# Kernel tuning notes

Hardware: AMD Instinct MI355X
Metric: run time of the kernel (lower is better)

Reference implementation:

```python
import jax, jax.numpy as jnp
import numpy as np

N = 4096          # leng_doc (number of tokens)
D_S = 70          # DEP_EMB_DIM + 2*BI_LSTM_PHASE_1_OUTPUT_DIM = 10 + 60

def setup_inputs() -> dict:
    key = jax.random.key(0)
    k1, k2 = jax.random.split(key)
    adj = jax.random.uniform(k1, (N, N, 2), dtype=jnp.float32)   # unweighted adjacency, 2 edge directions/channels
    s = jax.random.normal(k2, (N, D_S), dtype=jnp.float32)       # per-node edge-representation s
    return {"adj": adj, "s": s}

def reference(adj, s):
    # Faithful to CalculateHLayer-style math (CalculateSLayer analog):
    #   s_in[j,d]  = sum_i sum_k adj[i,j,k] * s[i,d]
    #   s_out[i,d] = sum_j sum_k adj[i,j,k] * s[j,d]
    # Sum over the channel axis k first, then contract the node axis with a GEMM
    # instead of materializing the (N,N,2,D) broadcast intermediate.
    a = adj.sum(axis=2)                 # (N, N)
    s_in = jnp.einsum('ij,id->jd', a, s)   # reduce over source nodes -> (N, D)
    s_out = jnp.einsum('ij,jd->id', a, s)  # reduce over target nodes -> (N, D)
    return (s_in, s_out)
```

## Files before the change

kernel.cpp:

```cpp
#include <hip/hip_runtime.h>


#define N    4096
#define D    70
#define DP   80
#define TILE 128
#define NT_D 5
#define NPART 32
#define ATP  132
#define SJP  136

typedef short short8  __attribute__((ext_vector_type(8)));
typedef short short4v __attribute__((ext_vector_type(4)));
typedef float f32x4   __attribute__((ext_vector_type(4)));

__device__ __forceinline__ unsigned short f2bf(float f) {
    unsigned u = __builtin_bit_cast(unsigned, f);
    u += 0x7FFFu + ((u >> 16) & 1u);
    return (unsigned short)(u >> 16);
}
__device__ __forceinline__ float bf2f(unsigned short h) {
    unsigned u = (unsigned)h << 16;
    return __builtin_bit_cast(float, u);
}
__device__ __forceinline__ short8 ld_b64x2(const unsigned short* p) {
    short4v lo = *(const short4v*)p;
    short4v hi = *(const short4v*)(p + 4);
    return __builtin_shufflevector(lo, hi, 0, 1, 2, 3, 4, 5, 6, 7);
}

__global__ __launch_bounds__(256) void build_sT(const float* __restrict__ s,
                                                unsigned short* __restrict__ sT) {
    __shared__ unsigned short tile[DP][264];
    const int t  = threadIdx.x;
    const int n0 = blockIdx.x * 256;
    #pragma unroll
    for (int d = 0; d < D; ++d)
        tile[d][t] = f2bf(s[(size_t)(n0 + t) * D + d]);
    __syncthreads();
    #pragma unroll
    for (int d = 0; d < DP; ++d) {
        unsigned short v = (d < D) ? tile[d][t] : (unsigned short)0;
        sT[(size_t)d * N + n0 + t] = v;
    }
}

template<bool USE_WS>
__global__ __launch_bounds__(512, 4) void fused_slayer(
    const float* __restrict__ adj,
    const unsigned short* __restrict__ sT,
    unsigned short* __restrict__ wsi,
    unsigned short* __restrict__ wso,
    float* __restrict__ out)
{
    __shared__ __align__(16) unsigned short a_row[2][TILE][40];
    __shared__ __align__(16) unsigned short aTt[2][32][ATP];
    __shared__ __align__(16) unsigned short sTj[DP][SJP];

    const int t    = threadIdx.x;
    const int lane = t & 63;
    const int w    = t >> 6;
    const int l16  = lane & 15;
    const int q    = lane >> 4;
    const int bx   = blockIdx.x;
    const int by   = blockIdx.y;
    const int I0   = by * TILE;
    const int J0   = bx * TILE;

    #pragma unroll
    for (int p = 0; p < 3; ++p) {
        int ii = t + 512 * p;
        if (ii < DP * 16) {
            int d = ii >> 4, c = ii & 15;
            *(uint4*)&sTj[d][8 * c] = *(const uint4*)(sT + (size_t)d * N + J0 + 8 * c);
        }
    }

    const int slot_mt = w & 1;
    const int slot_nt = w >> 1;
    const bool extra  = (w < 2);
    short8 bfi[4], bfe[4];
    {
        const int d = 16 * slot_nt + l16;
        #pragma unroll
        for (int ks = 0; ks < 4; ++ks)
            bfi[ks] = *(const short8*)(sT + (size_t)d * N + I0 + 32 * ks + 8 * q);
        if (extra) {
            const int d2 = 64 + l16;
            #pragma unroll
            for (int ks = 0; ks < 4; ++ks)
                bfe[ks] = *(const short8*)(sT + (size_t)d2 * N + I0 + 32 * ks + 8 * q);
        }
    }

    const f32x4 zero = {0.0f, 0.0f, 0.0f, 0.0f};
    f32x4 acc1[NT_D];
    #pragma unroll
    for (int nt = 0; nt < NT_D; ++nt) acc1[nt] = zero;

    const int jp = t & 15;
    const int ir = t >> 4;

    float4 v[4];
    #pragma unroll
    for (int it = 0; it < 4; ++it) {
        int i = 32 * it + ir;
        v[it] = *(const float4*)(adj + (size_t)(I0 + i) * (2 * N)
                                     + (size_t)(J0 + 2 * jp) * 2);
    }

    #pragma unroll
    for (int jc = 0; jc < 4; ++jc) {
        const int b = jc & 1;

        #pragma unroll
        for (int it = 0; it < 4; ++it) {
            int i = 32 * it + ir;
            unsigned short b0 = f2bf(v[it].x + v[it].y);
            unsigned short b1 = f2bf(v[it].z + v[it].w);
            *(unsigned int*)&a_row[b][i][2 * jp] =
                (unsigned int)b0 | ((unsigned int)b1 << 16);
            aTt[b][2 * jp][i]     = b0;
            aTt[b][2 * jp + 1][i] = b1;
        }
        __syncthreads();

        if (jc < 3) {
            #pragma unroll
            for (int it = 0; it < 4; ++it) {
                int i = 32 * it + ir;
                v[it] = *(const float4*)(adj + (size_t)(I0 + i) * (2 * N)
                                             + (size_t)(J0 + 32 * (jc + 1) + 2 * jp) * 2);
            }
        }

        {
            short8 af = *(const short8*)&a_row[b][16 * w + l16][8 * q];
            #pragma unroll
            for (int nt = 0; nt < NT_D; ++nt) {
                short8 bf = *(const short8*)&sTj[16 * nt + l16][32 * jc + 8 * q];
                acc1[nt] = __builtin_amdgcn_mfma_f32_16x16x32_bf16(af, bf, acc1[nt], 0, 0, 0);
            }
        }

        {
            f32x4 acc2 = zero;
            #pragma unroll
            for (int ks = 0; ks < 4; ++ks) {
                short8 af2 = ld_b64x2(&aTt[b][16 * slot_mt + l16][32 * ks + 8 * q]);
                acc2 = __builtin_amdgcn_mfma_f32_16x16x32_bf16(af2, bfi[ks], acc2, 0, 0, 0);
            }
            const int d = 16 * slot_nt + l16;
            #pragma unroll
            for (int r = 0; r < 4; ++r) {
                int gj = J0 + 32 * jc + 16 * slot_mt + 4 * q + r;
                if (USE_WS) {
                    wsi[((size_t)by * N + gj) * DP + d] = f2bf(acc2[r]);
                } else if (d < D) {
                    atomicAdd(&out[(size_t)gj * D + d], acc2[r]);
                }
            }
            if (extra) {
                f32x4 acc3 = zero;
                #pragma unroll
                for (int ks = 0; ks < 4; ++ks) {
                    short8 af3 = ld_b64x2(&aTt[b][16 * w + l16][32 * ks + 8 * q]);
                    acc3 = __builtin_amdgcn_mfma_f32_16x16x32_bf16(af3, bfe[ks], acc3, 0, 0, 0);
                }
                const int d2 = 64 + l16;
                #pragma unroll
                for (int r = 0; r < 4; ++r) {
                    int gj = J0 + 32 * jc + 16 * w + 4 * q + r;
                    if (USE_WS) {
                        wsi[((size_t)by * N + gj) * DP + d2] = f2bf(acc3[r]);
                    } else if (d2 < D) {
                        atomicAdd(&out[(size_t)gj * D + d2], acc3[r]);
                    }
                }
            }
        }
    }

    #pragma unroll
    for (int nt = 0; nt < NT_D; ++nt) {
        const int d = 16 * nt + l16;
        #pragma unroll
        for (int r = 0; r < 4; ++r) {
            int gi = I0 + 16 * w + 4 * q + r;
            if (USE_WS) {
                wso[((size_t)bx * N + gi) * DP + d] = f2bf(acc1[nt][r]);
            } else if (d < D) {
                atomicAdd(&out[(size_t)N * D + (size_t)gi * D + d], acc1[nt][r]);
            }
        }
    }
}

__global__ __launch_bounds__(128) void reduce_partials(
    const unsigned short* __restrict__ ws, float* __restrict__ out) {
    const int idx   = blockIdx.x * 128 + threadIdx.x;
    const int which = idx / (N * (DP / 8));
    const int rem   = idx % (N * (DP / 8));
    const int j     = rem / (DP / 8);
    const int g     = rem % (DP / 8);

    const unsigned short* base = ws + (size_t)which * ((size_t)NPART * N * DP)
                                    + (size_t)j * DP + 8 * g;
    float acc[8];
    #pragma unroll
    for (int e = 0; e < 8; ++e) acc[e] = 0.0f;
    #pragma unroll 8
    for (int p = 0; p < NPART; ++p) {
        short8 v = *(const short8*)(base + (size_t)p * N * DP);
        #pragma unroll
        for (int e = 0; e < 8; ++e)
            acc[e] += bf2f((unsigned short)v[e]);
    }

    float* o = out + (size_t)which * (N * D) + (size_t)j * D;
    #pragma unroll
    for (int e = 0; e < 8; ++e) {
        int d = 8 * g + e;
        if (d < D) o[d] = acc[e];
    }
}

extern "C" void kernel_launch(void* const* d_in, const int* in_sizes, int n_in,
                              void* d_out, int out_size, void* d_ws, size_t ws_size,
                              hipStream_t stream) {
    const float* adj = (const float*)d_in[0];
    const float* s   = (const float*)d_in[1];
    float* out = (float*)d_out;

    unsigned short* sT = (unsigned short*)d_ws;
    const size_t ST_BYTES   = (size_t)DP * N * sizeof(unsigned short);
    unsigned short* ws_part = (unsigned short*)((char*)d_ws + ST_BYTES);
    const size_t PART_ELEMS = (size_t)NPART * N * DP;
    const size_t NEED = ST_BYTES + 2 * PART_ELEMS * sizeof(unsigned short);

    build_sT<<<dim3(N / 256), dim3(256), 0, stream>>>(s, sT);

    if (ws_size >= NEED) {
        fused_slayer<true><<<dim3(N / TILE, N / TILE), dim3(512), 0, stream>>>(
            adj, sT, ws_part, ws_part + PART_ELEMS, out);
        reduce_partials<<<dim3(2 * N * (DP / 8) / 128), dim3(128), 0, stream>>>(
            ws_part, out);
    } else {
        hipMemsetAsync(d_out, 0, (size_t)2 * N * D * sizeof(float), stream);
        fused_slayer<false><<<dim3(N / TILE, N / TILE), dim3(512), 0, stream>>>(
            adj, sT, nullptr, nullptr, out);
    }
}
```

Baseline: 213.0 us.

## Double tile size to 256 and load s_j MFMA operands directly from global

Grows the fused block tile from 128x128 to 256x256, halving the number of partial sums written to workspace and reduced afterward (NPART 32 to 16), and doubling reuse of the register-resident s_i fragments. It drops the shared-memory staging of the s_j slice and reads those B operands straight from global/L2 each chunk. build_sT is also rewritten to transpose per-thread without shared memory. In exchange, register pressure rises (occupancy hint drops from 4 to 2 waves per SIMD) and the grid shrinks to 256 blocks, which may underfill the GPU.

```diff
diff --git a/kernel.cpp b/kernel.cpp
--- a/kernel.cpp
+++ b/kernel.cpp
@@ -4,11 +4,11 @@
 #define N    4096
 #define D    70
 #define DP   80
-#define TILE 128
+#define TILE 256
 #define NT_D 5
-#define NPART 32
-#define ATP  132
-#define SJP  136
+#define NPART 16
+#define ARP  40
+#define ATP  260
 
 typedef short short8  __attribute__((ext_vector_type(8)));
 typedef short short4v __attribute__((ext_vector_type(4)));
@@ -29,33 +29,34 @@
     return __builtin_shufflevector(lo, hi, 0, 1, 2, 3, 4, 5, 6, 7);
 }
 
-__global__ __launch_bounds__(256) void build_sT(const float* __restrict__ s,
+__global__ __launch_bounds__(128) void build_sT(const float* __restrict__ s,
                                                 unsigned short* __restrict__ sT) {
-    __shared__ unsigned short tile[DP][264];
     const int t  = threadIdx.x;
-    const int n0 = blockIdx.x * 256;
-    #pragma unroll
-    for (int d = 0; d < D; ++d)
-        tile[d][t] = f2bf(s[(size_t)(n0 + t) * D + d]);
-    __syncthreads();
-    #pragma unroll
-    for (int d = 0; d < DP; ++d) {
-        unsigned short v = (d < D) ? tile[d][t] : (unsigned short)0;
-        sT[(size_t)d * N + n0 + t] = v;
-    }
+    const int n  = blockIdx.x * 128 + t;
+    unsigned short col[DP];
+    #pragma unroll
+    for (int k = 0; k < D / 2; ++k) {
+        float2 v2 = *(const float2*)(s + (size_t)n * D + 2 * k);
+        col[2 * k]     = f2bf(v2.x);
+        col[2 * k + 1] = f2bf(v2.y);
+    }
+    #pragma unroll
+    for (int d = D; d < DP; ++d) col[d] = 0;
+    #pragma unroll
+    for (int d = 0; d < DP; ++d)
+        sT[(size_t)d * N + n] = col[d];
 }
 
 template<bool USE_WS>
-__global__ __launch_bounds__(512, 4) void fused_slayer(
+__global__ __launch_bounds__(512, 2) void fused_slayer(
     const float* __restrict__ adj,
     const unsigned short* __restrict__ sT,
     unsigned short* __restrict__ wsi,
     unsigned short* __restrict__ wso,
     float* __restrict__ out)
 {
-    __shared__ __align__(16) unsigned short a_row[2][TILE][40];
+    __shared__ __align__(16) unsigned short a_row[2][TILE][ARP];
     __shared__ __align__(16) unsigned short aTt[2][32][ATP];
-    __shared__ __align__(16) unsigned short sTj[DP][SJP];
 
     const int t    = threadIdx.x;
     const int lane = t & 63;
@@ -67,54 +68,47 @@
     const int I0   = by * TILE;
     const int J0   = bx * TILE;
 
-    #pragma unroll
-    for (int p = 0; p < 3; ++p) {
-        int ii = t + 512 * p;
-        if (ii < DP * 16) {
-            int d = ii >> 4, c = ii & 15;
-            *(uint4*)&sTj[d][8 * c] = *(const uint4*)(sT + (size_t)d * N + J0 + 8 * c);
-        }
-    }
-
     const int slot_mt = w & 1;
     const int slot_nt = w >> 1;
     const bool extra  = (w < 2);
-    short8 bfi[4], bfe[4];
+    short8 bfi[8], bfe[8];
     {
         const int d = 16 * slot_nt + l16;
         #pragma unroll
-        for (int ks = 0; ks < 4; ++ks)
+        for (int ks = 0; ks < 8; ++ks)
             bfi[ks] = *(const short8*)(sT + (size_t)d * N + I0 + 32 * ks + 8 * q);
         if (extra) {
             const int d2 = 64 + l16;
             #pragma unroll
-            for (int ks = 0; ks < 4; ++ks)
+            for (int ks = 0; ks < 8; ++ks)
                 bfe[ks] = *(const short8*)(sT + (size_t)d2 * N + I0 + 32 * ks + 8 * q);
         }
     }
 
     const f32x4 zero = {0.0f, 0.0f, 0.0f, 0.0f};
-    f32x4 acc1[NT_D];
-    #pragma unroll
-    for (int nt = 0; nt < NT_D; ++nt) acc1[nt] = zero;
+    f32x4 acc1[2][NT_D];
+    #pragma unroll
+    for (int h = 0; h < 2; ++h)
+        #pragma unroll
+        for (int nt = 0; nt < NT_D; ++nt) acc1[h][nt] = zero;
 
     const int jp = t & 15;
     const int ir = t >> 4;
 
-    float4 v[4];
-    #pragma unroll
-    for (int it = 0; it < 4; ++it) {
+    float4 v[8];
+    #pragma unroll
+    for (int it = 0; it < 8; ++it) {
         int i = 32 * it + ir;
         v[it] = *(const float4*)(adj + (size_t)(I0 + i) * (2 * N)
                                      + (size_t)(J0 + 2 * jp) * 2);
     }
 
-    #pragma unroll
-    for (int jc = 0; jc < 4; ++jc) {
+    #pragma unroll 2
+    for (int jc = 0; jc < 8; ++jc) {
         const int b = jc & 1;
 
         #pragma unroll
-        for (int it = 0; it < 4; ++it) {
+        for (int it = 0; it < 8; ++it) {
             int i = 32 * it + ir;
             unsigned short b0 = f2bf(v[it].x + v[it].y);
             unsigned short b1 = f2bf(v[it].z + v[it].w);
@@ -125,28 +119,25 @@
         }
         __syncthreads();
 
-        if (jc < 3) {
-            #pragma unroll
-            for (int it = 0; it < 4; ++it) {
+        if (jc < 7) {
+            #pragma unroll
+            for (int it = 0; it < 8; ++it) {
                 int i = 32 * it + ir;
                 v[it] = *(const float4*)(adj + (size_t)(I0 + i) * (2 * N)
                                              + (size_t)(J0 + 32 * (jc + 1) + 2 * jp) * 2);
             }
         }
 
-        {
-            short8 af = *(const short8*)&a_row[b][16 * w + l16][8 * q];
-            #pragma unroll
-            for (int nt = 0; nt < NT_D; ++nt) {
-                short8 bf = *(const short8*)&sTj[16 * nt + l16][32 * jc + 8 * q];
-                acc1[nt] = __builtin_amdgcn_mfma_f32_16x16x32_bf16(af, bf, acc1[nt], 0, 0, 0);
-            }
-        }
+        short8 bq[NT_D];
+        #pragma unroll
+        for (int nt = 0; nt < NT_D; ++nt)
+            bq[nt] = *(const short8*)(sT + (size_t)(16 * nt + l16) * N
+                                         + J0 + 32 * jc + 8 * q);
 
         {
             f32x4 acc2 = zero;
             #pragma unroll
-            for (int ks = 0; ks < 4; ++ks) {
+            for (int ks = 0; ks < 8; ++ks) {
                 short8 af2 = ld_b64x2(&aTt[b][16 * slot_mt + l16][32 * ks + 8 * q]);
                 acc2 = __builtin_amdgcn_mfma_f32_16x16x32_bf16(af2, bfi[ks], acc2, 0, 0, 0);
             }
@@ -163,7 +154,7 @@
             if (extra) {
                 f32x4 acc3 = zero;
                 #pragma unroll
-                for (int ks = 0; ks < 4; ++ks) {
+                for (int ks = 0; ks < 8; ++ks) {
                     short8 af3 = ld_b64x2(&aTt[b][16 * w + l16][32 * ks + 8 * q]);
                     acc3 = __builtin_amdgcn_mfma_f32_16x16x32_bf16(af3, bfe[ks], acc3, 0, 0, 0);
                 }
@@ -179,21 +170,31 @@
                 }
             }
         }
-    }
-
-    #pragma unroll
-    for (int nt = 0; nt < NT_D; ++nt) {
-        const int d = 16 * nt + l16;
-        #pragma unroll
-        for (int r = 0; r < 4; ++r) {
-            int gi = I0 + 16 * w + 4 * q + r;
-            if (USE_WS) {
-                wso[((size_t)bx * N + gi) * DP + d] = f2bf(acc1[nt][r]);
-            } else if (d < D) {
-                atomicAdd(&out[(size_t)N * D + (size_t)gi * D + d], acc1[nt][r]);
-            }
-        }
-    }
+
+        #pragma unroll
+        for (int h = 0; h < 2; ++h) {
+            short8 af = *(const short8*)&a_row[b][128 * h + 16 * w + l16][8 * q];
+            #pragma unroll
+            for (int nt = 0; nt < NT_D; ++nt)
+                acc1[h][nt] = __builtin_amdgcn_mfma_f32_16x16x32_bf16(af, bq[nt], acc1[h][nt], 0, 0, 0);
+        }
+    }
+
+    #pragma unroll
+    for (int h = 0; h < 2; ++h)
+        #pragma unroll
+        for (int nt = 0; nt < NT_D; ++nt) {
+            const int d = 16 * nt + l16;
+            #pragma unroll
+            for (int r = 0; r < 4; ++r) {
+                int gi = I0 + 128 * h + 16 * w + 4 * q + r;
+                if (USE_WS) {
+                    wso[((size_t)bx * N + gi) * DP + d] = f2bf(acc1[h][nt][r]);
+                } else if (d < D) {
+                    atomicAdd(&out[(size_t)N * D + (size_t)gi * D + d], acc1[h][nt][r]);
+                }
+            }
+        }
 }
 
 __global__ __launch_bounds__(128) void reduce_partials(
@@ -209,7 +210,7 @@
     float acc[8];
     #pragma unroll
     for (int e = 0; e < 8; ++e) acc[e] = 0.0f;
-    #pragma unroll 8
+    #pragma unroll
     for (int p = 0; p < NPART; ++p) {
         short8 v = *(const short8*)(base + (size_t)p * N * DP);
         #pragma unroll
@@ -238,7 +239,7 @@
     const size_t PART_ELEMS = (size_t)NPART * N * DP;
     const size_t NEED = ST_BYTES + 2 * PART_ELEMS * sizeof(unsigned short);
 
-    build_sT<<<dim3(N / 256), dim3(256), 0, stream>>>(s, sT);
+    build_sT<<<dim3(N / 128), dim3(128), 0, stream>>>(s, sT);
 
     if (ws_size >= NEED) {
         fused_slayer<true><<<dim3(N / TILE, N / TILE), dim3(512), 0, stream>>>(
```

Result: faster. 207.8 us (-2.4%).
